# Optimization experiments

Measured on AMD Instinct MI355X. Metric: run time of the kernel, lower is better.

Reference implementation:

```python
import jax, jax.numpy as jnp
import numpy as np

N_Q = 4; K = 4; IMG = 28; PAD = IMG + 2  # pad right/bottom so edge windows exist
N_WIN = 14 * 14  # stride-2 windows over 28x28


def _window_idx():
    # Faithful to torch: flatten the (possibly truncated) window row-major,
    # then pad with zeros AT THE END of the flattened vector.
    zero = PAD * PAD - 1  # padded image is zero there
    rows = []
    for i in range(0, IMG - 1, 2):
        for j in range(0, IMG - 1, 2):
            h = min(K, IMG - i); w = min(K, IMG - j)
            ids = [(i + r) * PAD + (j + c) for r in range(h) for c in range(w)]
            ids += [zero] * (K * K - len(ids))
            rows.append(ids)
    return np.asarray(rows, np.int32)  # [196, 16]

_WIDX = _window_idx()
# wire 0 is the most-significant bit of the 16-dim statevector index
_BITS = ((np.arange(16)[None, :] >> (3 - np.arange(4))[:, None]) & 1)
_ZSIGN = (1.0 - 2.0 * _BITS).astype(np.float32)  # [4, 16] PauliZ eigenvalues
# Four CRZ gates (control i, target (i+1)%4) are all diagonal -> combined diagonal phase
_CRZ_SIGNS = np.zeros(16, np.float32)
for _b in range(16):
    s = 0
    for _i in range(4):
        c = (_b >> (3 - _i)) & 1
        t = (_b >> (3 - ((_i + 1) % 4))) & 1
        s += c * (2 * t - 1)
    _CRZ_SIGNS[_b] = s
_H = (np.array([[1, 1], [1, -1]], np.complex64) / np.sqrt(2.0)).astype(np.complex64)


def _rz(a):  # a [B] -> [B,2,2]: diag(e^{-i a/2}, e^{+i a/2})
    em = jnp.exp(-0.5j * a); ep = jnp.exp(0.5j * a); z = jnp.zeros_like(em)
    return jnp.stack([jnp.stack([em, z], -1), jnp.stack([z, ep], -1)], -2)


def _ry(a):  # a [...] -> [...,2,2]
    c = jnp.cos(0.5 * a); s = jnp.sin(0.5 * a)
    return jnp.stack([jnp.stack([c, -s], -1), jnp.stack([s, c], -1)], -2).astype(jnp.complex64)


def _apply1q(state, U, w):  # state [B,16], U [B,2,2] or [2,2], wire w (0=MSB)
    L = 2 ** w; R = 2 ** (3 - w)
    s = state.reshape(-1, L, 2, R)
    if U.ndim == 2:
        out = jnp.einsum('ij,bajc->baic', U, s)
    else:
        out = jnp.einsum('bij,bajc->baic', U, s)
    return out.reshape(-1, 16)


def reference(x, crz_theta, ry_theta, fc1_w, fc1_b, fc2_w, fc2_b):
    B = x.shape[0]
    xp = jnp.pad(x[:, 0], ((0, 0), (0, 2), (0, 2))).reshape(B, -1)  # [B, 900]
    wins = xp[:, jnp.asarray(_WIDX)]              # [B, 196, 16]
    wins = jnp.transpose(wins, (1, 0, 2))         # [196, B, 16] for scan

    crz_diag = jnp.exp(0.5j * crz_theta * jnp.asarray(_CRZ_SIGNS))  # [16]
    Ry = _ry(ry_theta)                            # shared trainable RY, [2,2]
    H = jnp.asarray(_H)
    zsT = jnp.asarray(_ZSIGN).T                   # [16, 4]

    def step(state, f):  # state [B,16] complex64 persists ACROSS windows (no reset in source)
        for w in range(4):
            # compose H then the encoder rotations on this wire into one 2x2 per batch elem
            U = jnp.broadcast_to(H, (B, 2, 2))
            n = 5 if w < 3 else 1  # wire 3 only gets rz(f[15])
            for i in range(n):
                a = f[:, w * 5 + i]
                M = _rz(a) if i % 2 == 0 else _ry(a)  # gates = rz,ry,rz,ry,rz
                U = jnp.einsum('bij,bjk->bik', M, U)
            state = _apply1q(state, U, w)
        state = state * crz_diag[None, :]          # ring of CRZ gates (diagonal)
        for w in range(4):
            state = _apply1q(state, Ry, w)
        probs = state.real ** 2 + state.imag ** 2
        return state, probs @ zsT                  # [B, 4] PauliZ expectations

    state0 = jnp.zeros((B, 16), jnp.complex64).at[:, 0].set(1.0)
    _, outs = jax.lax.scan(step, state0, wins)     # [196, B, 4]
    feats = jnp.transpose(outs, (1, 0, 2)).reshape(B, N_WIN * 4)  # window-major concat
    h1 = feats @ fc1_w.T + fc1_b
    h1 = jnp.where(h1 > 0, h1, 0.1 * h1)           # LeakyReLU(0.1)
    return h1 @ fc2_w.T + fc2_b


def setup_inputs() -> dict:
    key = jax.random.key(0)
    ks = jax.random.split(key, 7)
    B = 16384
    return {
        'x': jax.random.normal(ks[0], (B, 1, 28, 28), jnp.float32),
        'crz_theta': jax.random.normal(ks[1], (), jnp.float32),
        'ry_theta': jax.random.normal(ks[2], (), jnp.float32),
        'fc1_w': jax.random.normal(ks[3], (20, 784), jnp.float32) * 0.03,
        'fc1_b': jnp.zeros((20,), jnp.float32),
        'fc2_w': jax.random.normal(ks[4], (2, 20), jnp.float32) * 0.1,
        'fc2_b': jnp.zeros((2,), jnp.float32),
    }
```

## Files before the change

kernel.cpp:

```cpp
#include <hip/hip_runtime.h>

#define RS2f 0.70710678118654752f

#define QP_XOR1 0xB1
#define QP_XOR2 0x4E
#define QP_BC0  0x00
#define QP_BC1  0x55
#define QP_BC2  0xAA
#define QP_BC3  0xFF

typedef float v2f __attribute__((ext_vector_type(2)));

template<int CTRL> __device__ __forceinline__ float dppf(float x) {
  return __int_as_float(__builtin_amdgcn_update_dpp(
      0, __float_as_int(x), CTRL, 0xF, 0xF, true));
}
template<int CTRL> __device__ __forceinline__ v2f dpp2(v2f v) {
  v2f r; r.x = dppf<CTRL>(v.x); r.y = dppf<CTRL>(v.y); return r;
}

__device__ __forceinline__ float sxor(float x, int sm) {
  return __int_as_float(__float_as_int(x) ^ sm);
}
__device__ __forceinline__ v2f vsplat(float a) { v2f r; r.x = a; r.y = a; return r; }
__device__ __forceinline__ v2f vperp(v2f v) { v2f r; r.x = -v.y; r.y = v.x; return r; }
__device__ __forceinline__ v2f vperc(v2f v) { v2f r; r.x = v.y; r.y = -v.x; return r; }
__device__ __forceinline__ v2f vfma2(float a, v2f b, v2f c) {
  return __builtin_elementwise_fma(vsplat(a), b, c);
}
__device__ __forceinline__ v2f vmul2(float a, v2f b) { return vsplat(a) * b; }

__device__ __forceinline__ void build_gate(float a0, float a1, float a2, float a3, float a4,
                                           float &w0r, float &w0i, float &w1r, float &w1i) {
  float sBp, cBp, sBm, cBm, sC, cC, sP, cP, sM, cM;
  __sincosf(0.5f * (a1 + a3), &sBp, &cBp);
  __sincosf(0.5f * (a1 - a3), &sBm, &cBm);
  __sincosf(0.5f * a2,        &sC,  &cC);
  __sincosf(0.5f * (a0 + a4), &sP,  &cP);
  __sincosf(0.5f * (a0 - a4), &sM,  &cM);
  float m00r =  cBp * cC, m00i = -cBm * sC;
  float m01r = -sBp * cC, m01i =  sBm * sC;
  float alr = fmaf(m00r, cP,  m00i * sP);
  float ali = fmaf(m00i, cP, -m00r * sP);
  float ber = fmaf(m01r, cM, -m01i * sM);
  float bei = fmaf(m01i, cM,  m01r * sM);
  w0r = RS2f * (alr + ber); w0i = RS2f * (ali + bei);
  w1r = RS2f * (alr - ber); w1i = RS2f * (ali - bei);
}

#define PICK_FULL                                                            \
  a0 = l0 ? P[0][0] : l1 ? P[1][1] : l2 ? P[2][2] : P[3][3];                 \
  a1 = l0 ? P[0][1] : l1 ? P[1][2] : l2 ? P[2][3] : 0.f;                     \
  a2 = l0 ? P[0][2] : l1 ? P[1][3] : l2 ? P[3][0] : 0.f;                     \
  a3 = l0 ? P[0][3] : l1 ? P[2][0] : l2 ? P[3][1] : 0.f;                     \
  a4 = l0 ? P[1][0] : l1 ? P[2][1] : l2 ? P[3][2] : 0.f;

#define PICK_W2                                                              \
  a0 = l0 ? P[0][0] : l1 ? P[2][1] : 0.f;                                    \
  a1 = l0 ? P[0][1] : l1 ? P[3][0] : 0.f;                                    \
  a2 = l0 ? P[1][0] : l1 ? P[3][1] : 0.f;                                    \
  a3 = l0 ? P[1][1] : 0.f;                                                   \
  a4 = l0 ? P[2][0] : 0.f;

#define PICK_H2                                                              \
  a0 = l0 ? P[0][0] : l1 ? P[1][1] : 0.f;                                    \
  a1 = l0 ? P[0][1] : l1 ? P[1][2] : 0.f;                                    \
  a2 = l0 ? P[0][2] : l1 ? P[1][3] : 0.f;                                    \
  a3 = l0 ? P[0][3] : 0.f;                                                   \
  a4 = l0 ? P[1][0] : 0.f;

#define PICK_22                                                              \
  a0 = l0 ? P[0][0] : 0.f;                                                   \
  a1 = l0 ? P[0][1] : 0.f;                                                   \
  a2 = l0 ? P[1][0] : 0.f;                                                   \
  a3 = l0 ? P[1][1] : 0.f;                                                   \
  a4 = 0.f;

#define APPLY_Z do {                                                         \
  { float w0r = dppf<QP_BC0>(Wc0), w0i = dppf<QP_BC0>(Wc1);                  \
    float w1r = dppf<QP_BC0>(Wc2), w1i = dppf<QP_BC0>(Wc3);                  \
    float uar = sxor(w0r, sm0), uai = w0i;                                   \
    float ubr = w1r,            ubi = sxor(w1i, sm0);                        \
    _Pragma("unroll")                                                        \
    for (int k = 0; k < 4; ++k) {                                            \
      v2f p = dpp2<QP_XOR2>(s[k]);                                           \
      v2f a = s[k];                                                          \
      s[k] = vfma2(uar, a, vfma2(uai, vperp(a),                              \
                   vfma2(ubr, p, vmul2(ubi, vperp(p)))));                    \
    } }                                                                      \
  { float w0r = dppf<QP_BC1>(Wc0), w0i = dppf<QP_BC1>(Wc1);                  \
    float w1r = dppf<QP_BC1>(Wc2), w1i = dppf<QP_BC1>(Wc3);                  \
    float uar = sxor(w0r, sm1), uai = w0i;                                   \
    float ubr = w1r,            ubi = sxor(w1i, sm1);                        \
    _Pragma("unroll")                                                        \
    for (int k = 0; k < 4; ++k) {                                            \
      v2f p = dpp2<QP_XOR1>(s[k]);                                           \
      v2f a = s[k];                                                          \
      s[k] = vfma2(uar, a, vfma2(uai, vperp(a),                              \
                   vfma2(ubr, p, vmul2(ubi, vperp(p)))));                    \
    } }                                                                      \
  { float w0r = dppf<QP_BC2>(Wc0), w0i = dppf<QP_BC2>(Wc1);                  \
    float w1r = dppf<QP_BC2>(Wc2), w1i = dppf<QP_BC2>(Wc3);                  \
    float nw0r = -w0r, nw0i = -w0i;                                          \
    _Pragma("unroll")                                                        \
    for (int k = 0; k < 2; ++k) {                                            \
      v2f lo = s[k], hi = s[k+2];                                            \
      s[k]   = vfma2(w0r, lo, vfma2(w0i, vperp(lo),                          \
                     vfma2(w1r, hi, vmul2(w1i, vperp(hi)))));                \
      s[k+2] = vfma2(w1r, lo, vfma2(w1i, vperc(lo),                          \
                     vfma2(nw0r, hi, vmul2(nw0i, vperc(hi)))));              \
    } }                                                                      \
  { float w0r = dppf<QP_BC3>(Wc0), w0i = dppf<QP_BC3>(Wc1);                  \
    float w1r = dppf<QP_BC3>(Wc2), w1i = dppf<QP_BC3>(Wc3);                  \
    float nw0r = -w0r, nw0i = -w0i;                                          \
    _Pragma("unroll")                                                        \
    for (int k = 0; k < 4; k += 2) {                                         \
      v2f lo = s[k], hi = s[k+1];                                            \
      s[k]   = vfma2(w0r, lo, vfma2(w0i, vperp(lo),                          \
                     vfma2(w1r, hi, vmul2(w1i, vperp(hi)))));                \
      s[k+1] = vfma2(w1r, lo, vfma2(w1i, vperc(lo),                          \
                     vfma2(nw0r, hi, vmul2(nw0i, vperc(hi)))));              \
    } }                                                                      \
  _Pragma("unroll")                                                          \
  for (int k = 0; k < 4; ++k)                                                \
    s[k] = vfma2(czk[k], s[k], vmul2(szk[k], vperp(s[k])));                  \
  _Pragma("unroll")                                                          \
  for (int k = 0; k < 4; ++k) {                                              \
    v2f p = dpp2<QP_XOR2>(s[k]);                                             \
    s[k] = vfma2(cry, s[k], vmul2(sgn0, p));                                 \
  }                                                                          \
  _Pragma("unroll")                                                          \
  for (int k = 0; k < 4; ++k) {                                              \
    v2f p = dpp2<QP_XOR1>(s[k]);                                             \
    s[k] = vfma2(cry, s[k], vmul2(sgn1, p));                                 \
  }                                                                          \
  _Pragma("unroll")                                                          \
  for (int k = 0; k < 2; ++k) {                                              \
    v2f lo = s[k], hi = s[k+2];                                              \
    s[k]   = vfma2(cry, lo, vmul2(nsry, hi));                                \
    s[k+2] = vfma2(sry, lo, vmul2(cry, hi));                                 \
  }                                                                          \
  _Pragma("unroll")                                                          \
  for (int k = 0; k < 4; k += 2) {                                           \
    v2f lo = s[k], hi = s[k+1];                                              \
    s[k]   = vfma2(cry, lo, vmul2(nsry, hi));                                \
    s[k+1] = vfma2(sry, lo, vmul2(cry, hi));                                 \
  }                                                                          \
  { v2f q0 = s[0]*s[0], q1 = s[1]*s[1], q2 = s[2]*s[2], q3 = s[3]*s[3];      \
    float p0 = q0.x + q0.y, p1 = q1.x + q1.y;                                \
    float p2 = q2.x + q2.y, p3 = q3.x + q3.y;                                \
    float s01 = p0 + p1, s23 = p2 + p3;                                      \
    float t_  = s01 + s23;                                                   \
    np0 = sxor(t_, sm0);                                                     \
    np1 = sxor(t_, sm1);                                                     \
    np2 = s01 - s23;                                                         \
    np3 = (p0 - p1) + (p2 - p3);                                             \
  }                                                                          \
} while (0)

#define BF_FOLD do {                                                         \
  float o0 = pd0, o1 = pd1, o2 = pd2, o3 = pd3;                              \
  o0 += dppf<QP_XOR1>(o0); o0 += dppf<QP_XOR2>(o0);                          \
  o1 += dppf<QP_XOR1>(o1); o1 += dppf<QP_XOR2>(o1);                          \
  o2 += dppf<QP_XOR1>(o2); o2 += dppf<QP_XOR2>(o2);                          \
  o3 += dppf<QP_XOR1>(o3); o3 += dppf<QP_XOR2>(o3);                          \
  const float* wp = swl + pdWin * 4;                                         \
  float4 wv0 = *(const float4*)(wp);                                         \
  float4 wv1 = *(const float4*)(wp + 784);                                   \
  float4 wv2 = *(const float4*)(wp + 1568);                                  \
  float4 wv3 = *(const float4*)(wp + 2352);                                  \
  float4 wv4 = *(const float4*)(wp + 3136);                                  \
  h1[0] = fmaf(wv0.x, o0, fmaf(wv0.y, o1, fmaf(wv0.z, o2, fmaf(wv0.w, o3, h1[0])))); \
  h1[1] = fmaf(wv1.x, o0, fmaf(wv1.y, o1, fmaf(wv1.z, o2, fmaf(wv1.w, o3, h1[1])))); \
  h1[2] = fmaf(wv2.x, o0, fmaf(wv2.y, o1, fmaf(wv2.z, o2, fmaf(wv2.w, o3, h1[2])))); \
  h1[3] = fmaf(wv3.x, o0, fmaf(wv3.y, o1, fmaf(wv3.z, o2, fmaf(wv3.w, o3, h1[3])))); \
  h1[4] = fmaf(wv4.x, o0, fmaf(wv4.y, o1, fmaf(wv4.z, o2, fmaf(wv4.w, o3, h1[4])))); \
} while (0)

#define SHIFT_PEND(WIN)  pd0 = np0; pd1 = np1; pd2 = np2; pd3 = np3; pdWin = (WIN);
#define ROTATE_W  Wc0 = Wn0; Wc1 = Wn1; Wc2 = Wn2; Wc3 = Wn3;

__global__ void __launch_bounds__(256)
quanv_kernel(const float* __restrict__ x,
             const float* __restrict__ crz_t,
             const float* __restrict__ ry_t,
             const float* __restrict__ fc1_w,
             const float* __restrict__ fc1_b,
             const float* __restrict__ fc2_w,
             const float* __restrict__ fc2_b,
             float* __restrict__ out, int B)
{
  __shared__ float sw[20 * 784];
  const int tid = threadIdx.x;
  for (int i = tid; i < (20 * 784) / 4; i += 256)
    ((float4*)sw)[i] = ((const float4*)fc1_w)[i];
  __syncthreads();

  const int l = tid & 3;
  const int b = (blockIdx.x * 256 + tid) >> 2;
  if (b >= B) return;
  const float* img = x + (size_t)b * 784;
  const bool l0 = (l == 0), l1 = (l == 1), l2 = (l == 2);

  const float theta = crz_t[0];
  const float ryt   = ry_t[0];
  float cry, sry;
  __sincosf(0.5f * ryt, &sry, &cry);
  const float nsry = -sry;
  const float sgn0 = (l & 2) ? sry : -sry;
  const float sgn1 = (l & 1) ? sry : -sry;
  const int sm0 = (l & 2) ? (int)0x80000000 : 0;
  const int sm1 = (l & 1) ? (int)0x80000000 : 0;

  float g0,g1,g2,g3;
  if      (l == 0) { g0= 0.f; g1=-1.f; g2=-1.f; g3=0.f; }
  else if (l == 1) { g0=-1.f; g1=-2.f; g2= 0.f; g3=1.f; }
  else if (l == 2) { g0=-1.f; g1= 0.f; g2=-2.f; g3=1.f; }
  else             { g0= 0.f; g1= 1.f; g2= 1.f; g3=4.f; }
  float czk[4], szk[4];
  __sincosf(0.5f*theta*g0, &szk[0], &czk[0]);
  __sincosf(0.5f*theta*g1, &szk[1], &czk[1]);
  __sincosf(0.5f*theta*g2, &szk[2], &czk[2]);
  __sincosf(0.5f*theta*g3, &szk[3], &czk[3]);

  v2f s[4];
#pragma unroll
  for (int k = 0; k < 4; ++k) { s[k].x = 0.f; s[k].y = 0.f; }
  if (l == 0) s[0].x = 1.f;

  float h1[5];
#pragma unroll
  for (int j = 0; j < 5; ++j) h1[j] = 0.f;
  const float* swl = sw + 5 * l * 784;

  float P[4][4];
  float a0, a1, a2, a3, a4;
  float Wc0, Wc1, Wc2, Wc3, Wn0, Wn1, Wn2, Wn3;
  float np0, np1, np2, np3;
  float pd0 = 0.f, pd1 = 0.f, pd2 = 0.f, pd3 = 0.f;
  int pdWin = 0;

#pragma unroll 1
  for (int wi = 0; wi < 13; ++wi) {
    const float* imgw = img + (2 * wi) * 28;

#pragma unroll
    for (int r = 0; r < 4; ++r) {
      float4 v = *(const float4*)(imgw + r * 28);
      P[r][0]=v.x; P[r][1]=v.y; P[r][2]=v.z; P[r][3]=v.w;
    }
    PICK_FULL;
    build_gate(a0, a1, a2, a3, a4, Wc0, Wc1, Wc2, Wc3);

    float2 Q0 = *(const float2*)(imgw + 0 * 28 + 4);
    float2 Q1 = *(const float2*)(imgw + 1 * 28 + 4);
    float2 Q2 = *(const float2*)(imgw + 2 * 28 + 4);
    float2 Q3 = *(const float2*)(imgw + 3 * 28 + 4);

#pragma unroll 4
    for (int wj = 1; wj <= 12; ++wj) {
      P[0][0]=P[0][2]; P[0][1]=P[0][3]; P[0][2]=Q0.x; P[0][3]=Q0.y;
      P[1][0]=P[1][2]; P[1][1]=P[1][3]; P[1][2]=Q1.x; P[1][3]=Q1.y;
      P[2][0]=P[2][2]; P[2][1]=P[2][3]; P[2][2]=Q2.x; P[2][3]=Q2.y;
      P[3][0]=P[3][2]; P[3][1]=P[3][3]; P[3][2]=Q3.x; P[3][3]=Q3.y;
      const int c0n = (wj < 12) ? (2 * wj + 4) : 24;
      Q0 = *(const float2*)(imgw + 0 * 28 + c0n);
      Q1 = *(const float2*)(imgw + 1 * 28 + c0n);
      Q2 = *(const float2*)(imgw + 2 * 28 + c0n);
      Q3 = *(const float2*)(imgw + 3 * 28 + c0n);
      PICK_FULL;
      build_gate(a0, a1, a2, a3, a4, Wn0, Wn1, Wn2, Wn3);
      APPLY_Z;
      BF_FOLD;
      SHIFT_PEND(wi * 14 + wj - 1);
      ROTATE_W;
    }

#pragma unroll
    for (int r = 0; r < 4; ++r) {
      P[r][0] = P[r][2]; P[r][1] = P[r][3]; P[r][2] = 0.f; P[r][3] = 0.f;
    }
    PICK_W2;
    build_gate(a0, a1, a2, a3, a4, Wn0, Wn1, Wn2, Wn3);
    APPLY_Z;
    BF_FOLD;
    SHIFT_PEND(wi * 14 + 12);
    ROTATE_W;
    APPLY_Z;
    BF_FOLD;
    SHIFT_PEND(wi * 14 + 13);
  }

  {
    const float* imgw = img + 26 * 28;
#pragma unroll
    for (int r = 0; r < 2; ++r) {
      float4 v = *(const float4*)(imgw + r * 28);
      P[r][0]=v.x; P[r][1]=v.y; P[r][2]=v.z; P[r][3]=v.w;
    }
#pragma unroll
    for (int r = 2; r < 4; ++r) { P[r][0]=0.f; P[r][1]=0.f; P[r][2]=0.f; P[r][3]=0.f; }
    PICK_H2;
    build_gate(a0, a1, a2, a3, a4, Wc0, Wc1, Wc2, Wc3);

    float2 Q0 = *(const float2*)(imgw + 4);
    float2 Q1 = *(const float2*)(imgw + 28 + 4);

#pragma unroll 4
    for (int wj = 1; wj <= 12; ++wj) {
      P[0][0]=P[0][2]; P[0][1]=P[0][3]; P[0][2]=Q0.x; P[0][3]=Q0.y;
      P[1][0]=P[1][2]; P[1][1]=P[1][3]; P[1][2]=Q1.x; P[1][3]=Q1.y;
      const int c0n = (wj < 12) ? (2 * wj + 4) : 24;
      Q0 = *(const float2*)(imgw + c0n);
      Q1 = *(const float2*)(imgw + 28 + c0n);
      PICK_H2;
      build_gate(a0, a1, a2, a3, a4, Wn0, Wn1, Wn2, Wn3);
      APPLY_Z;
      BF_FOLD;
      SHIFT_PEND(182 + wj - 1);
      ROTATE_W;
    }

    P[0][0]=P[0][2]; P[0][1]=P[0][3]; P[0][2]=0.f; P[0][3]=0.f;
    P[1][0]=P[1][2]; P[1][1]=P[1][3]; P[1][2]=0.f; P[1][3]=0.f;
    PICK_22;
    build_gate(a0, a1, a2, a3, a4, Wn0, Wn1, Wn2, Wn3);
    APPLY_Z;
    BF_FOLD;
    SHIFT_PEND(182 + 12);
    ROTATE_W;
    APPLY_Z;
    BF_FOLD;
    SHIFT_PEND(182 + 13);
  }

  BF_FOLD;

  float pa = 0.f, pb = 0.f;
#pragma unroll
  for (int j = 0; j < 5; ++j) {
    const int r = 5 * l + j;
    float v = h1[j] + fc1_b[r];
    v = (v > 0.f) ? v : 0.1f * v;
    pa = fmaf(fc2_w[r],      v, pa);
    pb = fmaf(fc2_w[20 + r], v, pb);
  }
  pa += dppf<QP_XOR1>(pa); pa += dppf<QP_XOR2>(pa);
  pb += dppf<QP_XOR1>(pb); pb += dppf<QP_XOR2>(pb);
  if (l == 0) {
    float2 res; res.x = pa + fc2_b[0]; res.y = pb + fc2_b[1];
    *(float2*)(out + (size_t)b * 2) = res;
  }
}

extern "C" void kernel_launch(void* const* d_in, const int* in_sizes, int n_in,
                              void* d_out, int out_size, void* d_ws, size_t ws_size,
                              hipStream_t stream) {
  const float* x      = (const float*)d_in[0];
  const float* crz_t  = (const float*)d_in[1];
  const float* ry_t   = (const float*)d_in[2];
  const float* fc1_w  = (const float*)d_in[3];
  const float* fc1_b  = (const float*)d_in[4];
  const float* fc2_w  = (const float*)d_in[5];
  const float* fc2_b  = (const float*)d_in[6];
  float* out = (float*)d_out;
  const int B = in_sizes[0] / 784;
  const int grid = (B * 4 + 255) / 256;
  quanv_kernel<<<grid, 256, 0, stream>>>(x, crz_t, ry_t, fc1_w, fc1_b,
                                         fc2_w, fc2_b, out, B);
}
```

Baseline: 222.3 us.

## Split each sample's statevector across eight lanes instead of four

Each batch sample's 16-amplitude statevector is now spread over 8 lanes with 2 amplitudes each, instead of 4 lanes with 4 each. The top qubit is exchanged between lane halves with ds_swizzle, and the remaining qubits shift to DPP xor patterns. The fc1 accumulation is split across the halves and reduced with a swizzle at the end. This doubles the thread count and cuts per-thread register and ALU work per sample, at the cost of twice the redundant image loads and gate building per sample, plus extra cross-lane traffic through swizzle.

Result: slower. 258.0 us (+16.1%).

```diff
diff --git a/kernel.cpp b/kernel.cpp
--- a/kernel.cpp
+++ b/kernel.cpp
@@ -17,6 +17,13 @@
 }
 template<int CTRL> __device__ __forceinline__ v2f dpp2(v2f v) {
   v2f r; r.x = dppf<CTRL>(v.x); r.y = dppf<CTRL>(v.y); return r;
+}
+
+__device__ __forceinline__ float swz4(float x) {
+  return __int_as_float(__builtin_amdgcn_ds_swizzle(__float_as_int(x), 0x101F));
+}
+__device__ __forceinline__ v2f swz4v(v2f v) {
+  v2f r; r.x = swz4(v.x); r.y = swz4(v.y); return r;
 }
 
 __device__ __forceinline__ float sxor(float x, int sm) {
@@ -79,82 +86,72 @@
 #define APPLY_Z do {                                                         \
   { float w0r = dppf<QP_BC0>(Wc0), w0i = dppf<QP_BC0>(Wc1);                  \
     float w1r = dppf<QP_BC0>(Wc2), w1i = dppf<QP_BC0>(Wc3);                  \
-    float uar = sxor(w0r, sm0), uai = w0i;                                   \
-    float ubr = w1r,            ubi = sxor(w1i, sm0);                        \
+    float uar = sxor(w0r, smH), uai = w0i;                                   \
+    float ubr = w1r,            ubi = sxor(w1i, smH);                        \
     _Pragma("unroll")                                                        \
-    for (int k = 0; k < 4; ++k) {                                            \
-      v2f p = dpp2<QP_XOR2>(s[k]);                                           \
-      v2f a = s[k];                                                          \
-      s[k] = vfma2(uar, a, vfma2(uai, vperp(a),                              \
+    for (int m = 0; m < 2; ++m) {                                            \
+      v2f p = swz4v(s[m]);                                                   \
+      v2f a = s[m];                                                          \
+      s[m] = vfma2(uar, a, vfma2(uai, vperp(a),                              \
                    vfma2(ubr, p, vmul2(ubi, vperp(p)))));                    \
     } }                                                                      \
   { float w0r = dppf<QP_BC1>(Wc0), w0i = dppf<QP_BC1>(Wc1);                  \
     float w1r = dppf<QP_BC1>(Wc2), w1i = dppf<QP_BC1>(Wc3);                  \
-    float uar = sxor(w0r, sm1), uai = w0i;                                   \
-    float ubr = w1r,            ubi = sxor(w1i, sm1);                        \
+    float uar = sxor(w0r, sm2), uai = w0i;                                   \
+    float ubr = w1r,            ubi = sxor(w1i, sm2);                        \
     _Pragma("unroll")                                                        \
-    for (int k = 0; k < 4; ++k) {                                            \
-      v2f p = dpp2<QP_XOR1>(s[k]);                                           \
-      v2f a = s[k];                                                          \
-      s[k] = vfma2(uar, a, vfma2(uai, vperp(a),                              \
+    for (int m = 0; m < 2; ++m) {                                            \
+      v2f p = dpp2<QP_XOR2>(s[m]);                                           \
+      v2f a = s[m];                                                          \
+      s[m] = vfma2(uar, a, vfma2(uai, vperp(a),                              \
                    vfma2(ubr, p, vmul2(ubi, vperp(p)))));                    \
     } }                                                                      \
   { float w0r = dppf<QP_BC2>(Wc0), w0i = dppf<QP_BC2>(Wc1);                  \
     float w1r = dppf<QP_BC2>(Wc2), w1i = dppf<QP_BC2>(Wc3);                  \
-    float nw0r = -w0r, nw0i = -w0i;                                          \
+    float uar = sxor(w0r, sm1), uai = w0i;                                   \
+    float ubr = w1r,            ubi = sxor(w1i, sm1);                        \
     _Pragma("unroll")                                                        \
-    for (int k = 0; k < 2; ++k) {                                            \
-      v2f lo = s[k], hi = s[k+2];                                            \
-      s[k]   = vfma2(w0r, lo, vfma2(w0i, vperp(lo),                          \
-                     vfma2(w1r, hi, vmul2(w1i, vperp(hi)))));                \
-      s[k+2] = vfma2(w1r, lo, vfma2(w1i, vperc(lo),                          \
-                     vfma2(nw0r, hi, vmul2(nw0i, vperc(hi)))));              \
+    for (int m = 0; m < 2; ++m) {                                            \
+      v2f p = dpp2<QP_XOR1>(s[m]);                                           \
+      v2f a = s[m];                                                          \
+      s[m] = vfma2(uar, a, vfma2(uai, vperp(a),                              \
+                   vfma2(ubr, p, vmul2(ubi, vperp(p)))));                    \
     } }                                                                      \
   { float w0r = dppf<QP_BC3>(Wc0), w0i = dppf<QP_BC3>(Wc1);                  \
     float w1r = dppf<QP_BC3>(Wc2), w1i = dppf<QP_BC3>(Wc3);                  \
     float nw0r = -w0r, nw0i = -w0i;                                          \
-    _Pragma("unroll")                                                        \
-    for (int k = 0; k < 4; k += 2) {                                         \
-      v2f lo = s[k], hi = s[k+1];                                            \
-      s[k]   = vfma2(w0r, lo, vfma2(w0i, vperp(lo),                          \
-                     vfma2(w1r, hi, vmul2(w1i, vperp(hi)))));                \
-      s[k+1] = vfma2(w1r, lo, vfma2(w1i, vperc(lo),                          \
-                     vfma2(nw0r, hi, vmul2(nw0i, vperc(hi)))));              \
-    } }                                                                      \
+    v2f lo = s[0], hi = s[1];                                                \
+    s[0] = vfma2(w0r, lo, vfma2(w0i, vperp(lo),                              \
+                 vfma2(w1r, hi, vmul2(w1i, vperp(hi)))));                    \
+    s[1] = vfma2(w1r, lo, vfma2(w1i, vperc(lo),                              \
+                 vfma2(nw0r, hi, vmul2(nw0i, vperc(hi))))); }                \
+  s[0] = vfma2(czk0, s[0], vmul2(szk0, vperp(s[0])));                        \
+  s[1] = vfma2(czk1, s[1], vmul2(szk1, vperp(s[1])));                        \
   _Pragma("unroll")                                                          \
-  for (int k = 0; k < 4; ++k)                                                \
-    s[k] = vfma2(czk[k], s[k], vmul2(szk[k], vperp(s[k])));                  \
-  _Pragma("unroll")                                                          \
-  for (int k = 0; k < 4; ++k) {                                              \
-    v2f p = dpp2<QP_XOR2>(s[k]);                                             \
-    s[k] = vfma2(cry, s[k], vmul2(sgn0, p));                                 \
+  for (int m = 0; m < 2; ++m) {                                              \
+    v2f p = swz4v(s[m]);                                                     \
+    s[m] = vfma2(cry, s[m], vmul2(sgn0, p));                                 \
   }                                                                          \
   _Pragma("unroll")                                                          \
-  for (int k = 0; k < 4; ++k) {                                              \
-    v2f p = dpp2<QP_XOR1>(s[k]);                                             \
-    s[k] = vfma2(cry, s[k], vmul2(sgn1, p));                                 \
+  for (int m = 0; m < 2; ++m) {                                              \
+    v2f p = dpp2<QP_XOR2>(s[m]);                                             \
+    s[m] = vfma2(cry, s[m], vmul2(sgn1, p));                                 \
   }                                                                          \
   _Pragma("unroll")                                                          \
-  for (int k = 0; k < 2; ++k) {                                              \
-    v2f lo = s[k], hi = s[k+2];                                              \
-    s[k]   = vfma2(cry, lo, vmul2(nsry, hi));                                \
-    s[k+2] = vfma2(sry, lo, vmul2(cry, hi));                                 \
+  for (int m = 0; m < 2; ++m) {                                              \
+    v2f p = dpp2<QP_XOR1>(s[m]);                                             \
+    s[m] = vfma2(cry, s[m], vmul2(sgn2, p));                                 \
   }                                                                          \
-  _Pragma("unroll")                                                          \
-  for (int k = 0; k < 4; k += 2) {                                           \
-    v2f lo = s[k], hi = s[k+1];                                              \
-    s[k]   = vfma2(cry, lo, vmul2(nsry, hi));                                \
-    s[k+1] = vfma2(sry, lo, vmul2(cry, hi));                                 \
-  }                                                                          \
-  { v2f q0 = s[0]*s[0], q1 = s[1]*s[1], q2 = s[2]*s[2], q3 = s[3]*s[3];      \
+  { v2f lo = s[0], hi = s[1];                                                \
+    s[0] = vfma2(cry, lo, vmul2(nsry, hi));                                  \
+    s[1] = vfma2(sry, lo, vmul2(cry, hi)); }                                 \
+  { v2f q0 = s[0]*s[0], q1 = s[1]*s[1];                                      \
     float p0 = q0.x + q0.y, p1 = q1.x + q1.y;                                \
-    float p2 = q2.x + q2.y, p3 = q3.x + q3.y;                                \
-    float s01 = p0 + p1, s23 = p2 + p3;                                      \
-    float t_  = s01 + s23;                                                   \
-    np0 = sxor(t_, sm0);                                                     \
-    np1 = sxor(t_, sm1);                                                     \
-    np2 = s01 - s23;                                                         \
-    np3 = (p0 - p1) + (p2 - p3);                                             \
+    float t_ = p0 + p1;                                                      \
+    np0 = sxor(t_, smH);                                                     \
+    np1 = sxor(t_, sm2);                                                     \
+    np2 = sxor(t_, sm1);                                                     \
+    np3 = p0 - p1;                                                           \
   }                                                                          \
 } while (0)
 
@@ -164,17 +161,21 @@
   o1 += dppf<QP_XOR1>(o1); o1 += dppf<QP_XOR2>(o1);                          \
   o2 += dppf<QP_XOR1>(o2); o2 += dppf<QP_XOR2>(o2);                          \
   o3 += dppf<QP_XOR1>(o3); o3 += dppf<QP_XOR2>(o3);                          \
+  float uA = hsel ? o0 : o2;          \
+  float uB = hsel ? o1 : o3;                                                 \
+  float fa = (hsel ? o2 : o0) + swz4(uA);                                    \
+  float fb = (hsel ? o3 : o1) + swz4(uB);                                    \
   const float* wp = swl + pdWin * 4;                                         \
-  float4 wv0 = *(const float4*)(wp);                                         \
-  float4 wv1 = *(const float4*)(wp + 784);                                   \
-  float4 wv2 = *(const float4*)(wp + 1568);                                  \
-  float4 wv3 = *(const float4*)(wp + 2352);                                  \
-  float4 wv4 = *(const float4*)(wp + 3136);                                  \
-  h1[0] = fmaf(wv0.x, o0, fmaf(wv0.y, o1, fmaf(wv0.z, o2, fmaf(wv0.w, o3, h1[0])))); \
-  h1[1] = fmaf(wv1.x, o0, fmaf(wv1.y, o1, fmaf(wv1.z, o2, fmaf(wv1.w, o3, h1[1])))); \
-  h1[2] = fmaf(wv2.x, o0, fmaf(wv2.y, o1, fmaf(wv2.z, o2, fmaf(wv2.w, o3, h1[2])))); \
-  h1[3] = fmaf(wv3.x, o0, fmaf(wv3.y, o1, fmaf(wv3.z, o2, fmaf(wv3.w, o3, h1[3])))); \
-  h1[4] = fmaf(wv4.x, o0, fmaf(wv4.y, o1, fmaf(wv4.z, o2, fmaf(wv4.w, o3, h1[4])))); \
+  float2 wv0 = *(const float2*)(wp);                                         \
+  float2 wv1 = *(const float2*)(wp + 784);                                   \
+  float2 wv2 = *(const float2*)(wp + 1568);                                  \
+  float2 wv3 = *(const float2*)(wp + 2352);                                  \
+  float2 wv4 = *(const float2*)(wp + 3136);                                  \
+  h1[0] = fmaf(wv0.x, fa, fmaf(wv0.y, fb, h1[0]));                           \
+  h1[1] = fmaf(wv1.x, fa, fmaf(wv1.y, fb, h1[1]));                           \
+  h1[2] = fmaf(wv2.x, fa, fmaf(wv2.y, fb, h1[2]));                           \
+  h1[3] = fmaf(wv3.x, fa, fmaf(wv3.y, fb, h1[3]));                           \
+  h1[4] = fmaf(wv4.x, fa, fmaf(wv4.y, fb, h1[4]));                           \
 } while (0)
 
 #define SHIFT_PEND(WIN)  pd0 = np0; pd1 = np1; pd2 = np2; pd3 = np3; pdWin = (WIN);
@@ -196,42 +197,43 @@
     ((float4*)sw)[i] = ((const float4*)fc1_w)[i];
   __syncthreads();
 
-  const int l = tid & 3;
-  const int b = (blockIdx.x * 256 + tid) >> 2;
+  const int l8   = tid & 7;
+  const int q    = l8 & 3;
+  const int hsel = l8 >> 2;
+  const int b = (blockIdx.x * 256 + tid) >> 3;
   if (b >= B) return;
   const float* img = x + (size_t)b * 784;
-  const bool l0 = (l == 0), l1 = (l == 1), l2 = (l == 2);
+  const bool l0 = (q == 0), l1 = (q == 1), l2 = (q == 2);
 
   const float theta = crz_t[0];
   const float ryt   = ry_t[0];
   float cry, sry;
   __sincosf(0.5f * ryt, &sry, &cry);
   const float nsry = -sry;
-  const float sgn0 = (l & 2) ? sry : -sry;
-  const float sgn1 = (l & 1) ? sry : -sry;
-  const int sm0 = (l & 2) ? (int)0x80000000 : 0;
-  const int sm1 = (l & 1) ? (int)0x80000000 : 0;
-
-  float g0,g1,g2,g3;
-  if      (l == 0) { g0= 0.f; g1=-1.f; g2=-1.f; g3=0.f; }
-  else if (l == 1) { g0=-1.f; g1=-2.f; g2= 0.f; g3=1.f; }
-  else if (l == 2) { g0=-1.f; g1= 0.f; g2=-2.f; g3=1.f; }
-  else             { g0= 0.f; g1= 1.f; g2= 1.f; g3=4.f; }
-  float czk[4], szk[4];
-  __sincosf(0.5f*theta*g0, &szk[0], &czk[0]);
-  __sincosf(0.5f*theta*g1, &szk[1], &czk[1]);
-  __sincosf(0.5f*theta*g2, &szk[2], &czk[2]);
-  __sincosf(0.5f*theta*g3, &szk[3], &czk[3]);
-
-  v2f s[4];
-#pragma unroll
-  for (int k = 0; k < 4; ++k) { s[k].x = 0.f; s[k].y = 0.f; }
-  if (l == 0) s[0].x = 1.f;
+  const float sgn0 = hsel    ? sry : -sry;
+  const float sgn1 = (q & 2) ? sry : -sry;
+  const float sgn2 = (q & 1) ? sry : -sry;
+  const int SBIT = (int)0x80000000;
+  const int smH = hsel    ? SBIT : 0;
+  const int sm2 = (q & 2) ? SBIT : 0;
+  const int sm1 = (q & 1) ? SBIT : 0;
+
+  const int B1b = (q >> 1) & 1, B2b = q & 1;
+  const int gb = hsel * (2 * B1b - 1) + B1b * (2 * B2b - 1);
+  const float g0f = (float)(gb - B2b);
+  const float g1f = (float)(gb + B2b + 2 * hsel - 1);
+  float czk0, szk0, czk1, szk1;
+  __sincosf(0.5f * theta * g0f, &szk0, &czk0);
+  __sincosf(0.5f * theta * g1f, &szk1, &czk1);
+
+  v2f s[2];
+  s[0].x = 0.f; s[0].y = 0.f; s[1].x = 0.f; s[1].y = 0.f;
+  if (l8 == 0) s[0].x = 1.f;
 
   float h1[5];
 #pragma unroll
   for (int j = 0; j < 5; ++j) h1[j] = 0.f;
-  const float* swl = sw + 5 * l * 784;
+  const float* swl = sw + 5 * q * 784 + 2 * hsel;
 
   float P[4][4];
   float a0, a1, a2, a3, a4;
@@ -336,10 +338,13 @@
 
   BF_FOLD;
 
+#pragma unroll
+  for (int j = 0; j < 5; ++j) h1[j] += swz4(h1[j]);
+
   float pa = 0.f, pb = 0.f;
 #pragma unroll
   for (int j = 0; j < 5; ++j) {
-    const int r = 5 * l + j;
+    const int r = 5 * q + j;
     float v = h1[j] + fc1_b[r];
     v = (v > 0.f) ? v : 0.1f * v;
     pa = fmaf(fc2_w[r],      v, pa);
@@ -347,7 +352,7 @@
   }
   pa += dppf<QP_XOR1>(pa); pa += dppf<QP_XOR2>(pa);
   pb += dppf<QP_XOR1>(pb); pb += dppf<QP_XOR2>(pb);
-  if (l == 0) {
+  if (l8 == 0) {
     float2 res; res.x = pa + fc2_b[0]; res.y = pb + fc2_b[1];
     *(float2*)(out + (size_t)b * 2) = res;
   }
@@ -365,7 +370,7 @@
   const float* fc2_b  = (const float*)d_in[6];
   float* out = (float*)d_out;
   const int B = in_sizes[0] / 784;
-  const int grid = (B * 4 + 255) / 256;
+  const int grid = (B * 8 + 255) / 256;
   quanv_kernel<<<grid, 256, 0, stream>>>(x, crz_t, ry_t, fc1_w, fc1_b,
                                          fc2_w, fc2_b, out, B);
 }
```
